# Performance work log

Hardware: AMD Instinct MI355X
Metric: run time of the kernel (lower is better)

## Reference

```python
import jax, jax.numpy as jnp
import numpy as np

# Static config (matches init_kwargs)
TAU = 0.25
D_MODEL = 256; H = 8; DK = 32          # d_keys = d_model // n_heads
M = 64                                  # nb_random_features
K = 16                                  # nb_gumbel_sample
B = 8; T = 64; N = 100
PATCH = 8; STRIDE = 8; PAD = 0
P = (T + PAD - PATCH) // STRIDE + 1     # num_patch = 8 == T' of x
L = P * N                               # flattened token count
HIDDEN_HALF = 128                       # hidden_dim // 2 for AdjAttention


def setup_inputs() -> dict:
    key = jax.random.key(0)
    ks = jax.random.split(key, 16)

    def lin(k, o, i, s=0.02):
        kw, kb = jax.random.split(k)
        return (jax.random.normal(kw, (o, i), jnp.float32) * s,
                jax.random.normal(kb, (o,), jnp.float32) * s)

    x = jax.random.normal(ks[0], (B, P, N, D_MODEL), jnp.float32)
    adj = jax.random.uniform(ks[1], (B, T, N, N), jnp.float32)

    Wq_w, Wq_b = lin(ks[2], H * DK, D_MODEL)
    Wk_w, Wk_b = lin(ks[3], H * DK, D_MODEL)
    Wv_w, Wv_b = lin(ks[4], H * DK, D_MODEL)
    Wo_w, Wo_b = lin(ks[5], D_MODEL, H * DK)
    fc_w, fc_b = lin(ks[6], HIDDEN_HALF, N * N)
    out_w, out_b = lin(ks[7], 1, HIDDEN_HALF)
    ln_g = jnp.ones((DK,), jnp.float32)
    ln_b = jnp.zeros((DK,), jnp.float32)

    # Performer random-feature projection (original: data-seeded orthogonal QR;
    # reference uses a fixed Gaussian draw as the given projection matrix).
    proj = jax.random.normal(ks[8], (M, DK), jnp.float32)

    # Gumbel noise: g = (-log(Exp(1) + eps) + eps) / tau, shape [B, L, H, K]
    e = jax.random.exponential(ks[9], (B, L, H, K), dtype=jnp.float32) + 1e-8
    gumbels = (-jnp.log(e) + 1e-8) / TAU

    return dict(x=x, adj=adj, Wq_w=Wq_w, Wq_b=Wq_b, Wk_w=Wk_w, Wk_b=Wk_b,
                Wv_w=Wv_w, Wv_b=Wv_b, Wo_w=Wo_w, Wo_b=Wo_b,
                ln_g=ln_g, ln_b=ln_b, fc_w=fc_w, fc_b=fc_b,
                out_w=out_w, out_b=out_b, proj=proj, gumbels=gumbels)


def _softmax_kernel(data, is_query, proj):
    # data: [B, L, H, DK], proj: [M, DK] -> phi(data): [B, L, H, M]
    data = data * (data.shape[-1] ** -0.25)
    dd = jnp.einsum('blhd,md->blhm', data, proj)
    diag = 0.5 * jnp.sum(data * data, axis=-1, keepdims=True)
    stab = jnp.max(dd, axis=-1, keepdims=True)
    if not is_query:
        stab = jnp.max(stab, axis=1, keepdims=True)  # also max over tokens for keys
    return (proj.shape[0] ** -0.5) * (jnp.exp(dd - diag - stab) + 1e-6)


def _forward(x, adj, Wq_w, Wq_b, Wk_w, Wk_b, Wv_w, Wv_b, Wo_w, Wo_b,
             ln_g, ln_b, fc_w, fc_b, out_w, out_b, proj, gumbels):
    Bq, Tp, Nn, Dm = x.shape
    xt = x.reshape(Bq, Tp * Nn, Dm)                       # [B, L, D]
    q = (xt @ Wq_w.T + Wq_b).reshape(Bq, -1, H, DK)
    k = (xt @ Wk_w.T + Wk_b).reshape(Bq, -1, H, DK)
    v = (xt @ Wv_w.T + Wv_b).reshape(Bq, -1, H, DK)

    # kernelized gumbel softmax attention (NodeFormer-style)
    s = 1.0 / np.sqrt(TAU)
    qp = _softmax_kernel(q * s, True, proj)               # [B, L, H, M]
    kp = _softmax_kernel(k * s, False, proj)              # [B, L, H, M]
    kg = kp[:, :, :, None, :] * jnp.exp(gumbels)[..., None]   # [B, L, H, K, M]
    kvs = jnp.einsum('blhkm,blhd->bhkmd', kg, v)          # [B, H, K, M, DK]
    z_num = jnp.einsum('blhm,bhkmd->blhkd', qp, kvs)      # [B, L, H, K, DK]
    z_den = jnp.einsum('blhm,bhkm->blhk', qp, jnp.sum(kg, axis=1)) + 1e-8
    z = jnp.mean(z_num / z_den[..., None], axis=3)        # [B, L, H, DK]

    # LayerNorm over d_keys
    mu = jnp.mean(z, axis=-1, keepdims=True)
    var = jnp.var(z, axis=-1, keepdims=True)
    z = (z - mu) * jax.lax.rsqrt(var + 1e-5) * ln_g + ln_b

    # Adj_Patch: stride == patch_len, padding == 0 -> plain reshape over T
    ap = adj.reshape(Bq, P, PATCH, Nn, Nn)                # [B, P, pl, N, N]
    # PatchAdjFusion / AdjAttention: softmax over patch_len
    flat = ap.reshape(Bq * P, PATCH, Nn * Nn)
    h1 = jax.nn.relu(flat @ fc_w.T + fc_b)
    w = jax.nn.softmax(h1 @ out_w.T + out_b, axis=1)      # [B*P, pl, 1]
    fused = jnp.sum(ap * w.reshape(Bq, P, PATCH, 1, 1), axis=2)   # [B, P, N, N]

    # construct_adj_optimized: block-diagonal [B, P*N, P*N]
    blockmask = jnp.eye(P, dtype=fused.dtype)
    adj_g = (fused[:, :, :, None, :] * blockmask[None, :, None, :, None]
             ).reshape(Bq, P * Nn, P * Nn)

    # relational bias: row L1-normalize then aggregate V (rb_order = 1)
    denom = jnp.clip(jnp.sum(jnp.abs(adj_g), axis=2, keepdims=True), 1e-12, None)
    adj_norm = adj_g / denom
    bias = (adj_norm @ v.reshape(Bq, P * Nn, H * DK)).reshape(Bq, P * Nn, H, DK)
    z = z + bias

    out = z.reshape(Bq, P * Nn, H * DK) @ Wo_w.T + Wo_b
    return out.reshape(Bq, Tp, Nn, Dm)


def reference(x, adj, Wq_w, Wq_b, Wk_w, Wk_b, Wv_w, Wv_b, Wo_w, Wo_b,
              ln_g, ln_b, fc_w, fc_b, out_w, out_b, proj, gumbels):
    return _forward(x, adj, Wq_w, Wq_b, Wk_w, Wk_b, Wv_w, Wv_b, Wo_w, Wo_b,
                    ln_g, ln_b, fc_w, fc_b, out_w, out_b, proj, gumbels)
```

## Files before the change

### kernel.cpp

```cpp
#include <hip/hip_runtime.h>
#include <cstdint>

constexpr int B = 8, P = 8, N = 100, D = 256, H = 8, DK = 32, M = 64, KG = 16;
constexpr int L = P * N;
constexpr int NN = N * N;
constexpr float PHI_SCALE = 0.8408964152537145f;
constexpr float MINV = 0.125f;
constexpr int ADJ_SPLIT = 8;
constexpr int KPAD = 10240;

typedef __attribute__((ext_vector_type(8))) short short8v;
typedef __attribute__((ext_vector_type(4))) float f32x4;
typedef __attribute__((ext_vector_type(4))) unsigned short us4;

__device__ __forceinline__ unsigned short f2b(float f) {
    unsigned u = __float_as_uint(f);
    unsigned r = 0x7fffu + ((u >> 16) & 1u);
    return (unsigned short)((u + r) >> 16);
}

__global__ __launch_bounds__(256) void convert_kernel(
    const float* __restrict__ adj, const float* __restrict__ fcw,
    unsigned short* __restrict__ adjb, unsigned short* __restrict__ fcwb)
{
    const int col = blockIdx.x * 256 + threadIdx.x;
    const int row = blockIdx.y;
    if (row < 512) {
        float v = (col < NN) ? adj[(long)row * NN + col] : 0.f;
        adjb[(long)row * KPAD + col] = f2b(v);
    } else {
        const int r = row - 512;
        float v = (col < NN) ? fcw[(long)r * NN + col] : 0.f;
        fcwb[(long)r * KPAD + col] = f2b(v);
    }
}

__global__ __launch_bounds__(256) void convert_xw_kernel(
    const float* __restrict__ x, const float* __restrict__ Wq,
    const float* __restrict__ Wk, const float* __restrict__ Wv,
    const float* __restrict__ Wo,
    unsigned short* __restrict__ xb, unsigned short* __restrict__ wqkvb,
    unsigned short* __restrict__ wob)
{
    const int j = blockIdx.x * 256 + threadIdx.x;
    if (j < 1638400) {
        xb[j] = f2b(x[j]);
    } else if (j < 1703936) {
        wqkvb[j - 1638400] = f2b(Wq[j - 1638400]);
    } else if (j < 1769472) {
        wqkvb[j - 1638400] = f2b(Wk[j - 1703936]);
    } else if (j < 1835008) {
        wqkvb[j - 1638400] = f2b(Wv[j - 1769472]);
    } else {
        wob[j - 1835008] = f2b(Wo[j - 1835008]);
    }
}

__global__ __launch_bounds__(256) void adjfc_mfma_kernel(
    const unsigned short* __restrict__ adjb, const unsigned short* __restrict__ fcwb,
    float* __restrict__ h1part)
{
    const int task = blockIdx.x * 4 + (threadIdx.x >> 6);
    const int kt = task & 7;
    const int nt = (task >> 3) & 7;
    const int mt = task >> 6;
    const int lane = threadIdx.x & 63;
    const int row = lane & 15;
    const int ko = (lane >> 4) * 8;
    const unsigned short* pa = adjb + (long)(mt * 16 + row) * KPAD + kt * 1280 + ko;
    const unsigned short* pb = fcwb + (long)(nt * 16 + row) * KPAD + kt * 1280 + ko;
    f32x4 acc = {0.f, 0.f, 0.f, 0.f};
    #pragma unroll 4
    for (int s = 0; s < 40; ++s) {
        short8v a = *reinterpret_cast<const short8v*>(pa);
        short8v b = *reinterpret_cast<const short8v*>(pb);
        acc = __builtin_amdgcn_mfma_f32_16x16x32_bf16(a, b, acc, 0, 0, 0);
        pa += 32; pb += 32;
    }
    const int c = nt * 16 + (lane & 15);
    const int rbase = mt * 16 + (lane >> 4) * 4;
    #pragma unroll
    for (int j = 0; j < 4; ++j) {
        int r = rbase + j;
        h1part[((long)kt * 512 + r) * 128 + c] = acc[j];
    }
}

__global__ __launch_bounds__(128) void wsm_kernel(
    const float* __restrict__ h1part, const float* __restrict__ fcb,
    const float* __restrict__ ow, const float* __restrict__ ob,
    float* __restrict__ wsm)
{
    __shared__ float part[8][2];
    const int bp = blockIdx.x;
    const int t = threadIdx.x;
    float owv = ow[t], bb = fcb[t];
    for (int pl = 0; pl < 8; ++pl) {
        float h = 0.f;
        for (int s = 0; s < ADJ_SPLIT; ++s)
            h += h1part[((long)s * 512 + bp * 8 + pl) * 128 + t];
        float v = fmaxf(h + bb, 0.f) * owv;
        #pragma unroll
        for (int off = 1; off < 64; off <<= 1) v += __shfl_xor(v, off);
        if ((t & 63) == 0) part[pl][t >> 6] = v;
    }
    __syncthreads();
    if (t == 0) {
        float lg[8], mx = -1e30f;
        for (int pl = 0; pl < 8; ++pl) {
            lg[pl] = part[pl][0] + part[pl][1] + ob[0];
            mx = fmaxf(mx, lg[pl]);
        }
        float s = 0.f;
        for (int pl = 0; pl < 8; ++pl) { lg[pl] = expf(lg[pl] - mx); s += lg[pl]; }
        for (int pl = 0; pl < 8; ++pl) wsm[bp * 8 + pl] = lg[pl] / s;
    }
}

__global__ __launch_bounds__(256) void qkv_mfma_kernel(
    const unsigned short* __restrict__ xb, const unsigned short* __restrict__ wqkvb,
    const float* __restrict__ bq, const float* __restrict__ bk,
    const float* __restrict__ bv,
    float* __restrict__ q, float* __restrict__ k, float* __restrict__ v)
{
    const int task = blockIdx.x * 4 + (threadIdx.x >> 6);
    const int nt = task % 48;
    const int mt = task / 48;
    const int lane = threadIdx.x & 63;
    const int row = lane & 15;
    const int ko = (lane >> 4) * 8;
    const unsigned short* pa = xb + (long)(mt * 16 + row) * 256 + ko;
    const unsigned short* pb = wqkvb + (long)(nt * 16 + row) * 256 + ko;
    f32x4 acc = {0.f, 0.f, 0.f, 0.f};
    #pragma unroll
    for (int s = 0; s < 8; ++s) {
        short8v a = *reinterpret_cast<const short8v*>(pa + s * 32);
        short8v b = *reinterpret_cast<const short8v*>(pb + s * 32);
        acc = __builtin_amdgcn_mfma_f32_16x16x32_bf16(a, b, acc, 0, 0, 0);
    }
    const int matid = nt >> 4;
    const int col = (nt & 15) * 16 + (lane & 15);
    float* outp = (matid == 0) ? q : ((matid == 1) ? k : v);
    const float* bp = (matid == 0) ? bq : ((matid == 1) ? bk : bv);
    const float bias = bp[col];
    const int rbase = mt * 16 + (lane >> 4) * 4;
    #pragma unroll
    for (int j = 0; j < 4; ++j)
        outp[(long)(rbase + j) * 256 + col] = acc[j] + bias;
}

__global__ __launch_bounds__(256) void phiqk_kernel(
    const float* __restrict__ qb, const float* __restrict__ kb,
    const float* __restrict__ proj,
    float* __restrict__ qp, float* __restrict__ ddout,
    float* __restrict__ diagout, float* __restrict__ partmax)
{
    __shared__ float ps[64 * 33];
    __shared__ float wmax[4];
    const int t = threadIdx.x;
    for (int j = t; j < 2048; j += 256) ps[(j >> 5) * 33 + (j & 31)] = proj[j];
    __syncthreads();
    const int bi = blockIdx.x;
    const bool isq = bi < 1600;
    const int rb = isq ? bi : bi - 1600;
    const int bh = rb / 25;
    const int b = bh >> 3, h = bh & 7;
    const int lbase = (rb % 25) * 32;
    const int wi = t >> 6;
    const int m = t & 63;
    const float* src = isq ? qb : kb;
    float rmax = -1e30f;
    for (int si = 0; si < 8; ++si) {
        const int l = lbase + si * 4 + wi;
        const float* ptr = src + (b * L + l) * 256 + h * 32;
        float dd = 0.f, diag = 0.f;
        #pragma unroll
        for (int d2 = 0; d2 < 32; ++d2) {
            float xv = ptr[d2] * PHI_SCALE;
            dd += xv * ps[m * 33 + d2];
            diag += xv * xv;
        }
        diag *= 0.5f;
        float s = dd;
        #pragma unroll
        for (int off = 1; off < 64; off <<= 1) s = fmaxf(s, __shfl_xor(s, off));
        const int group = (b * L + l) * 8 + h;
        if (isq) {
            qp[group * 64 + m] = MINV * (expf(dd - diag - s) + 1e-6f);
        } else {
            ddout[group * 64 + m] = dd;
            if (m == 0) diagout[group] = diag;
            rmax = fmaxf(rmax, s);
        }
    }
    if (!isq) {
        if (m == 0) wmax[wi] = rmax;
        __syncthreads();
        if (t == 0)
            partmax[rb] = fmaxf(fmaxf(wmax[0], wmax[1]), fmaxf(wmax[2], wmax[3]));
    }
}

__global__ __launch_bounds__(64) void kmax_kernel(
    const float* __restrict__ partmax, float* __restrict__ kmax)
{
    const int bh = blockIdx.x;
    const int t = threadIdx.x;
    float s = (t < 25) ? partmax[bh * 25 + t] : -1e30f;
    #pragma unroll
    for (int off = 1; off < 64; off <<= 1) s = fmaxf(s, __shfl_xor(s, off));
    if (t == 0) kmax[bh] = s;
}

__global__ __launch_bounds__(512) void kvs_kernel(
    const float* __restrict__ dd, const float* __restrict__ diagk,
    const float* __restrict__ kmax, const float* __restrict__ vb,
    const float* __restrict__ gum,
    float* __restrict__ kvspart, float* __restrict__ ksumpart, int nsplit)
{
    constexpr int TL = 64;
    __shared__ float kps[TL][64];
    __shared__ float vs[TL][32];
    __shared__ float egs[TL][8];
    const int bi = blockIdx.x;
    const int khalf = bi & 1;
    const int sp = (bi >> 1) % nsplit;
    const int bh = bi / (2 * nsplit);
    const int b = bh >> 3, h = bh & 7;
    const int lstart = sp * L / nsplit;
    const int lend = (sp + 1) * L / nsplit;
    const int t = threadIdx.x;
    const int kq = t >> 6;
    const int mg = (t >> 3) & 7;
    const int dg = t & 7;
    const float stab = kmax[bh];
    float acc[8][4];
    #pragma unroll
    for (int i = 0; i < 8; ++i)
        for (int j = 0; j < 4; ++j) acc[i][j] = 0.f;
    float sacc[8] = {0, 0, 0, 0, 0, 0, 0, 0};
    for (int l0 = lstart; l0 < lend; l0 += TL) {
        const int chunk = min(TL, lend - l0);
        __syncthreads();
        for (int j = t; j < chunk * 64; j += 512) {
            int ll = j >> 6, m = j & 63;
            int g = (b * L + l0 + ll) * 8 + h;
            kps[ll][m] = MINV * (expf(dd[g * 64 + m] - diagk[g] - stab) + 1e-6f);
        }
        for (int j = t; j < chunk * 32; j += 512) {
            int ll = j >> 5;
            vs[ll][j & 31] = vb[(b * L + l0 + ll) * 256 + h * 32 + (j & 31)];
        }
        for (int j = t; j < chunk * 8; j += 512) {
            int ll = j >> 3;
            egs[ll][j & 7] = expf(gum[((b * L + l0 + ll) * 8 + h) * 16 + khalf * 8 + (j & 7)]);
        }
        __syncthreads();
        #pragma unroll 2
        for (int ll = 0; ll < chunk; ++ll) {
            float egv = egs[ll][kq];
            const float4* kr = reinterpret_cast<const float4*>(&kps[ll][mg * 8]);
            float4 ka = kr[0], kb4 = kr[1];
            float4 v4 = *reinterpret_cast<const float4*>(&vs[ll][dg * 4]);
            float s[8];
            s[0] = ka.x * egv;  s[1] = ka.y * egv;  s[2] = ka.z * egv;  s[3] = ka.w * egv;
            s[4] = kb4.x * egv; s[5] = kb4.y * egv; s[6] = kb4.z * egv; s[7] = kb4.w * egv;
            #pragma unroll
            for (int mi = 0; mi < 8; ++mi) {
                acc[mi][0] += s[mi] * v4.x;
                acc[mi][1] += s[mi] * v4.y;
                acc[mi][2] += s[mi] * v4.z;
                acc[mi][3] += s[mi] * v4.w;
            }
            if (dg == 0) {
                #pragma unroll
                for (int mi = 0; mi < 8; ++mi) sacc[mi] += s[mi];
            }
        }
    }
    const int k = khalf * 8 + kq;
    float* kbase = kvspart + (((long)(sp * 64 + bh) * 16 + k) * 64 + mg * 8) * 32 + dg * 4;
    #pragma unroll
    for (int mi = 0; mi < 8; ++mi)
        *reinterpret_cast<float4*>(kbase + mi * 32) =
            make_float4(acc[mi][0], acc[mi][1], acc[mi][2], acc[mi][3]);
    if (dg == 0) {
        float* sb = ksumpart + ((long)(sp * 64 + bh) * 16 + k) * 64 + mg * 8;
        #pragma unroll
        for (int mi = 0; mi < 8; ++mi) sb[mi] = sacc[mi];
    }
}

__global__ __launch_bounds__(256) void kvsreduce_kernel(
    const float* __restrict__ kvspart, const float* __restrict__ ksumpart,
    float* __restrict__ kvs, float* __restrict__ ksum, int nsplit)
{
    constexpr int NKVS4 = 2097152 / 4;
    constexpr int NKS = 65536;
    const int idx = blockIdx.x * 256 + threadIdx.x;
    if (idx < NKVS4) {
        const float4* p = reinterpret_cast<const float4*>(kvspart) + idx;
        float4 a = p[0];
        for (int s = 1; s < nsplit; ++s) {
            float4 b4 = p[(long)s * NKVS4];
            a.x += b4.x; a.y += b4.y; a.z += b4.z; a.w += b4.w;
        }
        reinterpret_cast<float4*>(kvs)[idx] = a;
    } else if (idx < NKVS4 + NKS) {
        int j = idx - NKVS4;
        float s = ksumpart[j];
        for (int sp = 1; sp < nsplit; ++sp) s += ksumpart[(long)sp * NKS + j];
        ksum[j] = s;
    }
}

__global__ __launch_bounds__(320) void z_kernel(
    const float* __restrict__ qp, const float* __restrict__ kvs,
    const float* __restrict__ ksum, const float* __restrict__ ln_g,
    const float* __restrict__ ln_b, float* __restrict__ z)
{
    __shared__ float qps[80][65];
    __shared__ float kvss[2048];
    __shared__ float ksums[16][65];
    __shared__ float invden[80][17];
    const int bi = blockIdx.x;
    const int bh = bi / 10;
    const int b = bh >> 3, h = bh & 7;
    const int l0 = (bi % 10) * 80;
    const int t = threadIdx.x;
    for (int j = t; j < 80 * 64; j += 320) {
        int ll = j >> 6;
        qps[ll][j & 63] = qp[((b * L + l0 + ll) * 8 + h) * 64 + (j & 63)];
    }
    for (int j = t; j < 16 * 64; j += 320)
        ksums[j >> 6][j & 63] = ksum[(long)bh * 1024 + j];
    __syncthreads();
    for (int j = t; j < 80 * 16; j += 320) {
        int ll = j >> 4, kk = j & 15;
        float s = 0.f;
        #pragma unroll 8
        for (int m = 0; m < 64; ++m) s += qps[ll][m] * ksums[kk][m];
        invden[ll][kk] = 1.0f / (s + 1e-8f);
    }
    const int lg = t >> 3;
    const int dg = t & 7;
    const int r0 = lg * 2, r1 = r0 + 1;
    float acc0[4] = {0, 0, 0, 0}, acc1[4] = {0, 0, 0, 0};
    for (int kk = 0; kk < 16; ++kk) {
        __syncthreads();
        const float4* src = reinterpret_cast<const float4*>(kvs + ((long)bh * 16 + kk) * 2048);
        for (int j = t; j < 512; j += 320)
            reinterpret_cast<float4*>(kvss)[j] = src[j];
        __syncthreads();
        float n0[4] = {0, 0, 0, 0}, n1[4] = {0, 0, 0, 0};
        #pragma unroll 4
        for (int m = 0; m < 64; ++m) {
            float4 k4 = *reinterpret_cast<const float4*>(&kvss[m * 32 + dg * 4]);
            float q0 = qps[r0][m], q1 = qps[r1][m];
            n0[0] += q0 * k4.x; n0[1] += q0 * k4.y; n0[2] += q0 * k4.z; n0[3] += q0 * k4.w;
            n1[0] += q1 * k4.x; n1[1] += q1 * k4.y; n1[2] += q1 * k4.z; n1[3] += q1 * k4.w;
        }
        float i0 = invden[r0][kk], i1 = invden[r1][kk];
        #pragma unroll
        for (int j = 0; j < 4; ++j) { acc0[j] += n0[j] * i0; acc1[j] += n1[j] * i1; }
    }
    const float4 g4 = reinterpret_cast<const float4*>(ln_g)[dg];
    const float4 b4 = reinterpret_cast<const float4*>(ln_b)[dg];
    #pragma unroll
    for (int ri = 0; ri < 2; ++ri) {
        float* a = ri ? acc1 : acc0;
        float zv[4];
        float s1 = 0.f, s2 = 0.f;
        #pragma unroll
        for (int j = 0; j < 4; ++j) {
            zv[j] = a[j] * (1.0f / 16.0f);
            s1 += zv[j]; s2 += zv[j] * zv[j];
        }
        #pragma unroll
        for (int off = 1; off < 8; off <<= 1) {
            s1 += __shfl_xor(s1, off);
            s2 += __shfl_xor(s2, off);
        }
        float mu = s1 * (1.0f / 32.0f);
        float var = s2 * (1.0f / 32.0f) - mu * mu;
        float rs = rsqrtf(var + 1e-5f);
        float4 o;
        o.x = (zv[0] - mu) * rs * g4.x + b4.x;
        o.y = (zv[1] - mu) * rs * g4.y + b4.y;
        o.z = (zv[2] - mu) * rs * g4.z + b4.z;
        o.w = (zv[3] - mu) * rs * g4.w + b4.w;
        const int r = ri ? r1 : r0;
        *reinterpret_cast<float4*>(&z[(b * L + l0 + r) * 256 + h * 32 + dg * 4]) = o;
    }
}

__global__ __launch_bounds__(128) void fused_kernel(
    const float* __restrict__ adj, const float* __restrict__ wsm,
    float* __restrict__ fusedn)
{
    __shared__ float part[2];
    const int bi = blockIdx.x;
    const int b = bi / 800;
    const int p = (bi / 100) & 7;
    const int i = bi % 100;
    const int t = threadIdx.x;
    float f = 0.f;
    if (t < 100) {
        #pragma unroll
        for (int pl = 0; pl < 8; ++pl)
            f += adj[((long)(b * 64 + p * 8 + pl)) * NN + i * 100 + t] * wsm[(b * 8 + p) * 8 + pl];
    }
    float a = fabsf(f);
    #pragma unroll
    for (int off = 1; off < 64; off <<= 1) a += __shfl_xor(a, off);
    if ((t & 63) == 0) part[t >> 6] = a;
    __syncthreads();
    float denom = fmaxf(part[0] + part[1], 1e-12f);
    if (t < 100) fusedn[(long)bi * 100 + t] = f / denom;
}

__global__ __launch_bounds__(256) void bias_kernel(
    const float* __restrict__ fusedn, const float* __restrict__ vb,
    float* __restrict__ z)
{
    __shared__ float fs[10 * 100];
    const int bi = blockIdx.x;
    const int bp = bi / 10;
    const int b = bp >> 3, p = bp & 7;
    const int i0 = (bi % 10) * 10;
    const int t = threadIdx.x;
    for (int j = t; j < 1000; j += 256)
        fs[j] = fusedn[(long)bp * 10000 + i0 * 100 + j];
    __syncthreads();
    float acc[10];
    #pragma unroll
    for (int r = 0; r < 10; ++r) acc[r] = 0.f;
    for (int j = 0; j < 100; ++j) {
        float vj = vb[(b * 800 + p * 100 + j) * 256 + t];
        #pragma unroll
        for (int r = 0; r < 10; ++r)
            acc[r] += fs[r * 100 + j] * vj;
    }
    for (int r = 0; r < 10; ++r)
        z[(b * 800 + p * 100 + i0 + r) * 256 + t] += acc[r];
}

__global__ __launch_bounds__(256) void convert_z_kernel(
    const float* __restrict__ z, unsigned short* __restrict__ zb)
{
    const int i = (blockIdx.x * 256 + threadIdx.x) * 4;
    float4 v = *reinterpret_cast<const float4*>(z + i);
    us4 o = { f2b(v.x), f2b(v.y), f2b(v.z), f2b(v.w) };
    *reinterpret_cast<us4*>(zb + i) = o;
}

__global__ __launch_bounds__(256) void out_mfma_kernel(
    const unsigned short* __restrict__ zb, const unsigned short* __restrict__ wob,
    const float* __restrict__ bo, float* __restrict__ out)
{
    const int task = blockIdx.x * 4 + (threadIdx.x >> 6);
    const int nt = task & 15;
    const int mt = task >> 4;
    const int lane = threadIdx.x & 63;
    const int row = lane & 15;
    const int ko = (lane >> 4) * 8;
    const unsigned short* pa = zb + (long)(mt * 16 + row) * 256 + ko;
    const unsigned short* pb = wob + (long)(nt * 16 + row) * 256 + ko;
    f32x4 acc = {0.f, 0.f, 0.f, 0.f};
    #pragma unroll
    for (int s = 0; s < 8; ++s) {
        short8v a = *reinterpret_cast<const short8v*>(pa + s * 32);
        short8v b = *reinterpret_cast<const short8v*>(pb + s * 32);
        acc = __builtin_amdgcn_mfma_f32_16x16x32_bf16(a, b, acc, 0, 0, 0);
    }
    const int col = nt * 16 + (lane & 15);
    const float bias = bo[col];
    const int rbase = mt * 16 + (lane >> 4) * 4;
    #pragma unroll
    for (int j = 0; j < 4; ++j)
        out[(long)(rbase + j) * 256 + col] = acc[j] + bias;
}

extern "C" void kernel_launch(void* const* d_in, const int* in_sizes, int n_in,
                              void* d_out, int out_size, void* d_ws, size_t ws_size,
                              hipStream_t stream) {
    const float* x     = (const float*)d_in[0];
    const float* adj   = (const float*)d_in[1];
    const float* Wq_w  = (const float*)d_in[2];
    const float* Wq_b  = (const float*)d_in[3];
    const float* Wk_w  = (const float*)d_in[4];
    const float* Wk_b  = (const float*)d_in[5];
    const float* Wv_w  = (const float*)d_in[6];
    const float* Wv_b  = (const float*)d_in[7];
    const float* Wo_w  = (const float*)d_in[8];
    const float* Wo_b  = (const float*)d_in[9];
    const float* ln_g  = (const float*)d_in[10];
    const float* ln_b  = (const float*)d_in[11];
    const float* fc_w  = (const float*)d_in[12];
    const float* fc_b  = (const float*)d_in[13];
    const float* out_w = (const float*)d_in[14];
    const float* out_b = (const float*)d_in[15];
    const float* proj  = (const float*)d_in[16];
    const float* gum   = (const float*)d_in[17];
    float* out = (float*)d_out;

    float* ws = (float*)d_ws;
    const size_t wsfl = ws_size / sizeof(float);
    constexpr size_t AFTER_NEED = 11260032;
    const int nsplit = (wsfl >= (size_t)6 * 2162688 + AFTER_NEED) ? 6 : 3;
    const size_t OVL = (size_t)nsplit * 2162688;

    float* ovl = ws;
    unsigned short* adjb = (unsigned short*)ovl;
    unsigned short* fcwb = (unsigned short*)(ovl + 2621440);
    float* h1part  = ovl + 3276800;
    float* qbuf    = ovl;
    float* kbuf    = ovl + 1638400;
    unsigned short* xb    = (unsigned short*)(ovl + 3276800);
    unsigned short* wqkvb = (unsigned short*)(ovl + 4096000);
    float* kvspart = ovl;
    float* ksumpart= ovl + (size_t)nsplit * 2097152;
    float* zbuf    = ovl;
    float* fusedn  = ovl + 1638400;

    float* after   = ws + OVL;
    float* vbuf    = after;
    float* qp      = vbuf + 1638400;
    float* kp      = qp + 3276800;
    float* diagk   = kp + 3276800;
    float* kvs     = diagk + 51200;
    float* ksum    = kvs + 2097152;
    float* wsm     = ksum + 65536;
    float* partmax = wsm + 512;
    float* kmax    = partmax + 1600;
    unsigned short* wob  = (unsigned short*)(kmax + 64);
    unsigned short* zb16 = (unsigned short*)(kmax + 64 + 32768);

    convert_kernel<<<dim3(40, 640), 256, 0, stream>>>(adj, fc_w, adjb, fcwb);
    adjfc_mfma_kernel<<<512, 256, 0, stream>>>(adjb, fcwb, h1part);
    wsm_kernel<<<64, 128, 0, stream>>>(h1part, fc_b, out_w, out_b, wsm);

    convert_xw_kernel<<<7424, 256, 0, stream>>>(x, Wq_w, Wk_w, Wv_w, Wo_w,
                                                xb, wqkvb, wob);
    qkv_mfma_kernel<<<4800, 256, 0, stream>>>(xb, wqkvb, Wq_b, Wk_b, Wv_b,
                                              qbuf, kbuf, vbuf);
    phiqk_kernel<<<3200, 256, 0, stream>>>(qbuf, kbuf, proj, qp, kp, diagk, partmax);
    kmax_kernel<<<64, 64, 0, stream>>>(partmax, kmax);
    kvs_kernel<<<64 * nsplit * 2, 512, 0, stream>>>(kp, diagk, kmax, vbuf, gum,
                                                    kvspart, ksumpart, nsplit);
    kvsreduce_kernel<<<2304, 256, 0, stream>>>(kvspart, ksumpart, kvs, ksum, nsplit);
    z_kernel<<<640, 320, 0, stream>>>(qp, kvs, ksum, ln_g, ln_b, zbuf);
    fused_kernel<<<6400, 128, 0, stream>>>(adj, wsm, fusedn);
    bias_kernel<<<640, 256, 0, stream>>>(fusedn, vbuf, zbuf);
    convert_z_kernel<<<1600, 256, 0, stream>>>(zbuf, zb16);
    out_mfma_kernel<<<1600, 256, 0, stream>>>(zb16, wob, Wo_b, out);
}
```

Measured before the change: 453.5 us.

## Split kvs and z kernels into smaller blocks and fuse z bf16 conversion into bias

kvs_kernel now uses 256-thread blocks that each cover 4 gumbel samples instead of 8, which doubles the grid. z_kernel processes 40 rows per block with one row per thread group instead of 80, also doubling the grid. bias_kernel now writes bf16 z directly, so the separate convert_z kernel and its read-modify-write of z are gone. The aim is more parallel blocks and one fewer launch and memory pass. The cost is that kvs blocks recompute the exp of K features twice as often, and z blocks reload kvs tiles twice as often.

```diff
diff --git a/kernel.cpp b/kernel.cpp
--- a/kernel.cpp
+++ b/kernel.cpp
@@ -212,7 +212,7 @@
     if (t == 0) kmax[bh] = s;
 }
 
-__global__ __launch_bounds__(512) void kvs_kernel(
+__global__ __launch_bounds__(256) void kvs_kernel(
     const float* __restrict__ dd, const float* __restrict__ diagk,
     const float* __restrict__ kmax, const float* __restrict__ vb,
     const float* __restrict__ gum,
@@ -221,16 +221,16 @@
     constexpr int TL = 64;
     __shared__ float kps[TL][64];
     __shared__ float vs[TL][32];
-    __shared__ float egs[TL][8];
+    __shared__ float egs[TL][4];
     const int bi = blockIdx.x;
-    const int khalf = bi & 1;
-    const int sp = (bi >> 1) % nsplit;
-    const int bh = bi / (2 * nsplit);
+    const int kq4 = bi & 3;
+    const int sp = (bi >> 2) % nsplit;
+    const int bh = bi / (4 * nsplit);
     const int b = bh >> 3, h = bh & 7;
     const int lstart = sp * L / nsplit;
     const int lend = (sp + 1) * L / nsplit;
     const int t = threadIdx.x;
-    const int kq = t >> 6;
+    const int kw = t >> 6;
     const int mg = (t >> 3) & 7;
     const int dg = t & 7;
     const float stab = kmax[bh];
@@ -242,23 +242,23 @@
     for (int l0 = lstart; l0 < lend; l0 += TL) {
         const int chunk = min(TL, lend - l0);
         __syncthreads();
-        for (int j = t; j < chunk * 64; j += 512) {
+        for (int j = t; j < chunk * 64; j += 256) {
             int ll = j >> 6, m = j & 63;
             int g = (b * L + l0 + ll) * 8 + h;
             kps[ll][m] = MINV * (expf(dd[g * 64 + m] - diagk[g] - stab) + 1e-6f);
         }
-        for (int j = t; j < chunk * 32; j += 512) {
+        for (int j = t; j < chunk * 32; j += 256) {
             int ll = j >> 5;
             vs[ll][j & 31] = vb[(b * L + l0 + ll) * 256 + h * 32 + (j & 31)];
         }
-        for (int j = t; j < chunk * 8; j += 512) {
-            int ll = j >> 3;
-            egs[ll][j & 7] = expf(gum[((b * L + l0 + ll) * 8 + h) * 16 + khalf * 8 + (j & 7)]);
+        for (int j = t; j < chunk * 4; j += 256) {
+            int ll = j >> 2;
+            egs[ll][j & 3] = expf(gum[((b * L + l0 + ll) * 8 + h) * 16 + kq4 * 4 + (j & 3)]);
         }
         __syncthreads();
         #pragma unroll 2
         for (int ll = 0; ll < chunk; ++ll) {
-            float egv = egs[ll][kq];
+            float egv = egs[ll][kw];
             const float4* kr = reinterpret_cast<const float4*>(&kps[ll][mg * 8]);
             float4 ka = kr[0], kb4 = kr[1];
             float4 v4 = *reinterpret_cast<const float4*>(&vs[ll][dg * 4]);
@@ -278,7 +278,7 @@
             }
         }
     }
-    const int k = khalf * 8 + kq;
+    const int k = kq4 * 4 + kw;
     float* kbase = kvspart + (((long)(sp * 64 + bh) * 16 + k) * 64 + mg * 8) * 32 + dg * 4;
     #pragma unroll
     for (int mi = 0; mi < 8; ++mi)
@@ -319,79 +319,72 @@
     const float* __restrict__ ksum, const float* __restrict__ ln_g,
     const float* __restrict__ ln_b, float* __restrict__ z)
 {
-    __shared__ float qps[80][65];
+    __shared__ float qps[40][65];
     __shared__ float kvss[2048];
     __shared__ float ksums[16][65];
-    __shared__ float invden[80][17];
+    __shared__ float invden[40][17];
     const int bi = blockIdx.x;
-    const int bh = bi / 10;
+    const int bh = bi / 20;
     const int b = bh >> 3, h = bh & 7;
-    const int l0 = (bi % 10) * 80;
-    const int t = threadIdx.x;
-    for (int j = t; j < 80 * 64; j += 320) {
+    const int l0 = (bi % 20) * 40;
+    const int t = threadIdx.x;
+    for (int j = t; j < 40 * 64; j += 320) {
         int ll = j >> 6;
         qps[ll][j & 63] = qp[((b * L + l0 + ll) * 8 + h) * 64 + (j & 63)];
     }
     for (int j = t; j < 16 * 64; j += 320)
         ksums[j >> 6][j & 63] = ksum[(long)bh * 1024 + j];
     __syncthreads();
-    for (int j = t; j < 80 * 16; j += 320) {
+    for (int j = t; j < 40 * 16; j += 320) {
         int ll = j >> 4, kk = j & 15;
         float s = 0.f;
         #pragma unroll 8
         for (int m = 0; m < 64; ++m) s += qps[ll][m] * ksums[kk][m];
         invden[ll][kk] = 1.0f / (s + 1e-8f);
     }
-    const int lg = t >> 3;
+    const int lr = t >> 3;
     const int dg = t & 7;
-    const int r0 = lg * 2, r1 = r0 + 1;
-    float acc0[4] = {0, 0, 0, 0}, acc1[4] = {0, 0, 0, 0};
+    float acc[4] = {0, 0, 0, 0};
     for (int kk = 0; kk < 16; ++kk) {
         __syncthreads();
         const float4* src = reinterpret_cast<const float4*>(kvs + ((long)bh * 16 + kk) * 2048);
         for (int j = t; j < 512; j += 320)
             reinterpret_cast<float4*>(kvss)[j] = src[j];
         __syncthreads();
-        float n0[4] = {0, 0, 0, 0}, n1[4] = {0, 0, 0, 0};
+        float n[4] = {0, 0, 0, 0};
         #pragma unroll 4
         for (int m = 0; m < 64; ++m) {
             float4 k4 = *reinterpret_cast<const float4*>(&kvss[m * 32 + dg * 4]);
-            float q0 = qps[r0][m], q1 = qps[r1][m];
-            n0[0] += q0 * k4.x; n0[1] += q0 * k4.y; n0[2] += q0 * k4.z; n0[3] += q0 * k4.w;
-            n1[0] += q1 * k4.x; n1[1] += q1 * k4.y; n1[2] += q1 * k4.z; n1[3] += q1 * k4.w;
-        }
-        float i0 = invden[r0][kk], i1 = invden[r1][kk];
-        #pragma unroll
-        for (int j = 0; j < 4; ++j) { acc0[j] += n0[j] * i0; acc1[j] += n1[j] * i1; }
+            float qv = qps[lr][m];
+            n[0] += qv * k4.x; n[1] += qv * k4.y; n[2] += qv * k4.z; n[3] += qv * k4.w;
+        }
+        float iv = invden[lr][kk];
+        #pragma unroll
+        for (int j = 0; j < 4; ++j) acc[j] += n[j] * iv;
     }
     const float4 g4 = reinterpret_cast<const float4*>(ln_g)[dg];
     const float4 b4 = reinterpret_cast<const float4*>(ln_b)[dg];
-    #pragma unroll
-    for (int ri = 0; ri < 2; ++ri) {
-        float* a = ri ? acc1 : acc0;
-        float zv[4];
-        float s1 = 0.f, s2 = 0.f;
-        #pragma unroll
-        for (int j = 0; j < 4; ++j) {
-            zv[j] = a[j] * (1.0f / 16.0f);
-            s1 += zv[j]; s2 += zv[j] * zv[j];
-        }
-        #pragma unroll
-        for (int off = 1; off < 8; off <<= 1) {
-            s1 += __shfl_xor(s1, off);
-            s2 += __shfl_xor(s2, off);
-        }
-        float mu = s1 * (1.0f / 32.0f);
-        float var = s2 * (1.0f / 32.0f) - mu * mu;
-        float rs = rsqrtf(var + 1e-5f);
-        float4 o;
-        o.x = (zv[0] - mu) * rs * g4.x + b4.x;
-        o.y = (zv[1] - mu) * rs * g4.y + b4.y;
-        o.z = (zv[2] - mu) * rs * g4.z + b4.z;
-        o.w = (zv[3] - mu) * rs * g4.w + b4.w;
-        const int r = ri ? r1 : r0;
-        *reinterpret_cast<float4*>(&z[(b * L + l0 + r) * 256 + h * 32 + dg * 4]) = o;
-    }
+    float zv[4];
+    float s1 = 0.f, s2 = 0.f;
+    #pragma unroll
+    for (int j = 0; j < 4; ++j) {
+        zv[j] = acc[j] * (1.0f / 16.0f);
+        s1 += zv[j]; s2 += zv[j] * zv[j];
+    }
+    #pragma unroll
+    for (int off = 1; off < 8; off <<= 1) {
+        s1 += __shfl_xor(s1, off);
+        s2 += __shfl_xor(s2, off);
+    }
+    float mu = s1 * (1.0f / 32.0f);
+    float var = s2 * (1.0f / 32.0f) - mu * mu;
+    float rs = rsqrtf(var + 1e-5f);
+    float4 o;
+    o.x = (zv[0] - mu) * rs * g4.x + b4.x;
+    o.y = (zv[1] - mu) * rs * g4.y + b4.y;
+    o.z = (zv[2] - mu) * rs * g4.z + b4.z;
+    o.w = (zv[3] - mu) * rs * g4.w + b4.w;
+    *reinterpret_cast<float4*>(&z[(b * L + l0 + lr) * 256 + h * 32 + dg * 4]) = o;
 }
 
 __global__ __launch_bounds__(128) void fused_kernel(
@@ -421,7 +414,7 @@
 
 __global__ __launch_bounds__(256) void bias_kernel(
     const float* __restrict__ fusedn, const float* __restrict__ vb,
-    float* __restrict__ z)
+    const float* __restrict__ z, unsigned short* __restrict__ zb16)
 {
     __shared__ float fs[10 * 100];
     const int bi = blockIdx.x;
@@ -441,17 +434,10 @@
         for (int r = 0; r < 10; ++r)
             acc[r] += fs[r * 100 + j] * vj;
     }
-    for (int r = 0; r < 10; ++r)
-        z[(b * 800 + p * 100 + i0 + r) * 256 + t] += acc[r];
-}
-
-__global__ __launch_bounds__(256) void convert_z_kernel(
-    const float* __restrict__ z, unsigned short* __restrict__ zb)
-{
-    const int i = (blockIdx.x * 256 + threadIdx.x) * 4;
-    float4 v = *reinterpret_cast<const float4*>(z + i);
-    us4 o = { f2b(v.x), f2b(v.y), f2b(v.z), f2b(v.w) };
-    *reinterpret_cast<us4*>(zb + i) = o;
+    for (int r = 0; r < 10; ++r) {
+        const long idx = (long)(b * 800 + p * 100 + i0 + r) * 256 + t;
+        zb16[idx] = f2b(z[idx] + acc[r]);
+    }
 }
 
 __global__ __launch_bounds__(256) void out_mfma_kernel(
@@ -546,12 +532,11 @@
                                               qbuf, kbuf, vbuf);
     phiqk_kernel<<<3200, 256, 0, stream>>>(qbuf, kbuf, proj, qp, kp, diagk, partmax);
     kmax_kernel<<<64, 64, 0, stream>>>(partmax, kmax);
-    kvs_kernel<<<64 * nsplit * 2, 512, 0, stream>>>(kp, diagk, kmax, vbuf, gum,
+    kvs_kernel<<<64 * nsplit * 4, 256, 0, stream>>>(kp, diagk, kmax, vbuf, gum,
                                                     kvspart, ksumpart, nsplit);
     kvsreduce_kernel<<<2304, 256, 0, stream>>>(kvspart, ksumpart, kvs, ksum, nsplit);
-    z_kernel<<<640, 320, 0, stream>>>(qp, kvs, ksum, ln_g, ln_b, zbuf);
+    z_kernel<<<1280, 320, 0, stream>>>(qp, kvs, ksum, ln_g, ln_b, zbuf);
     fused_kernel<<<6400, 128, 0, stream>>>(adj, wsm, fusedn);
-    bias_kernel<<<640, 256, 0, stream>>>(fusedn, vbuf, zbuf);
-    convert_z_kernel<<<1600, 256, 0, stream>>>(zbuf, zb16);
+    bias_kernel<<<640, 256, 0, stream>>>(fusedn, vbuf, zbuf, zb16);
     out_mfma_kernel<<<1600, 256, 0, stream>>>(zb16, wob, Wo_b, out);
 }
```

Result: slower. 505.0 us (+11.4%).
